# Kernel tuning notes

Measured on AMD Instinct MI355X. Metric: run time of the kernel, lower is better.

The kernel has to match this reference:

```python
import jax, jax.numpy as jnp
import numpy as np

jax.config.update("jax_enable_x64", True)  # module does int64 wraparound hashing

# Derived from BloomFilter(num_items=10_000_000, false_positive_rate=0.01):
#   pre-round num_bits = ceil(1e7 * ln(100) / ln(2)^2) ~= 95,850,584
#   num_hashes = ceil(pre_round_bits / 1e7 * ln(2)) = 7
#   num_bits rounded up to power of two -> 2**27
NUM_BITS = 2 ** 27
BIT_MASK = NUM_BITS - 1
NUM_HASHES = 7
PRIME = 2654435761


def _hash(values):
    """(N,) int64 -> (N, k) bit positions. Matches torch: (v*PRIME + seed) & bit_mask
    (note Python precedence: & binds looser than +). int64 overflow wraps identically."""
    seeds = jnp.arange(NUM_HASHES, dtype=jnp.int64)
    return (values[:, None] * PRIME + seeds[None, :]) & BIT_MASK


def setup_inputs() -> dict:
    key = jax.random.key(0)
    k1, k2 = jax.random.split(key)
    add_values = jax.random.randint(k1, (4_000_000,), 0, 2**31 - 1, dtype=jnp.int64)
    query_values = jax.random.randint(k2, (8_000_000,), 0, 2**31 - 1, dtype=jnp.int64)
    return {"add_values": add_values, "query_values": query_values}


def reference(add_values, query_values):
    # Bit array of NUM_BITS bools. Semantically identical to the packed int64
    # bitset: word w, offset b in torch <-> flat index (w << 6) | b here, and a
    # bitwise-OR of single-bit masks is exactly an idempotent set-True scatter.
    bits = jnp.zeros((NUM_BITS,), dtype=bool)

    # add(): scatter-set all k hash positions of every inserted value
    add_pos = _hash(add_values)  # (M, k)
    bits = bits.at[add_pos.reshape(-1)].set(True)

    # contains(): gather k bits per query and AND-reduce
    q_pos = _hash(query_values)  # (N, k)
    return jnp.all(bits[q_pos], axis=1)  # (N,) bool
```

## Files before the change

### kernel.cpp

```cpp
#include <hip/hip_runtime.h>
#include <stdint.h>


#define NUM_BITS_LOG2 27
#define NUM_BITS (1u << NUM_BITS_LOG2)
#define BIT_MASK (NUM_BITS - 1u)
#define NUM_WORDS (NUM_BITS >> 6)
#define WORD_MASK (NUM_WORDS - 1u)
#define PRIME 2654435761u
#define H_WORDS (NUM_WORDS >> 2)

#define NBUCKETS 512
#define BKT_SHIFT (NUM_BITS_LOG2 - 9)
#define REGION_WORDS (1u << (BKT_SHIFT - 6))
#define H_WORDS_PER_REGION (REGION_WORDS / 4)
#define CAP 8688u
#define CHUNK 8192u

typedef int vint4 __attribute__((ext_vector_type(4)));
typedef unsigned long long vull2 __attribute__((ext_vector_type(2)));

#define WS_H_ONLY 20971520ull
#define WS_FULL   38766592ull

__global__ __launch_bounds__(512) void init_gcnt_kernel(uint32_t* __restrict__ gcnt) {
    gcnt[threadIdx.x] = 0u;
}

__global__ __launch_bounds__(512) void scatter_kernel(
    const int* __restrict__ vals, int n,
    uint32_t* __restrict__ lists, uint32_t* __restrict__ gcnt)
{
    __shared__ uint32_t hist[NBUCKETS];
    __shared__ uint32_t cur[NBUCKETS];
    __shared__ uint32_t gdelta[NBUCKETS];
    __shared__ uint32_t wsum[8];
    __shared__ uint32_t wexc[8];
    __shared__ uint32_t total_s;
    __shared__ uint32_t sortbuf[CHUNK];
    const uint32_t tid = threadIdx.x;
    const uint32_t lane = tid & 63u;
    const uint32_t wv = tid >> 6;
    const uint32_t un = (uint32_t)n;
    const uint32_t nchunks = (un + CHUNK - 1u) / CHUNK;

    for (uint32_t c = blockIdx.x; c < nchunks; c += gridDim.x) {
        const uint32_t base = c * CHUNK;
        const bool full = (base + CHUNK <= un);

        hist[tid] = 0u;
        __syncthreads();

        vint4 vv[4];
        if (full) {
            const vint4* src = (const vint4*)(vals + base);
            #pragma unroll
            for (int k = 0; k < 4; ++k) vv[k] = src[(uint32_t)k * 512u + tid];
            #pragma unroll
            for (int k = 0; k < 4; ++k) {
                #pragma unroll
                for (int j = 0; j < 4; ++j) {
                    uint32_t p = ((uint32_t)vv[k][j] * PRIME) & BIT_MASK;
                    uint32_t b1 = p >> BKT_SHIFT;
                    atomicAdd(&hist[b1], 1u);
                    uint32_t b2 = ((p + 6u) & BIT_MASK) >> BKT_SHIFT;
                    if (b2 != b1) {
                        uint32_t s2 = atomicAdd(&gcnt[b2], 1u);
                        if (s2 < CAP) lists[b2 * CAP + s2] = p;
                    }
                }
            }
        } else {
            #pragma unroll
            for (int k = 0; k < 16; ++k) {
                uint32_t idx = base + (uint32_t)k * 512u + tid;
                if (idx < un) {
                    uint32_t p = ((uint32_t)vals[idx] * PRIME) & BIT_MASK;
                    uint32_t b1 = p >> BKT_SHIFT;
                    atomicAdd(&hist[b1], 1u);
                    uint32_t b2 = ((p + 6u) & BIT_MASK) >> BKT_SHIFT;
                    if (b2 != b1) {
                        uint32_t s2 = atomicAdd(&gcnt[b2], 1u);
                        if (s2 < CAP) lists[b2 * CAP + s2] = p;
                    }
                }
            }
        }
        __syncthreads();

        const uint32_t c0 = hist[tid];
        uint32_t x = c0;
        #pragma unroll
        for (uint32_t d = 1; d < 64; d <<= 1) {
            uint32_t y = __shfl_up(x, d, 64);
            if (lane >= d) x += y;
        }
        if (lane == 63u) wsum[wv] = x;
        __syncthreads();
        if (wv == 0) {
            uint32_t t8 = (lane < 8u) ? wsum[lane] : 0u;
            #pragma unroll
            for (uint32_t d = 1; d < 8; d <<= 1) {
                uint32_t y = __shfl_up(t8, d, 64);
                if (lane >= d) t8 += y;
            }
            if (lane < 8u) wexc[lane] = t8 - wsum[lane];
        }
        __syncthreads();
        const uint32_t inc = x + wexc[wv];
        const uint32_t lb = inc - c0;
        if (tid == NBUCKETS - 1) total_s = inc;

        uint32_t go = c0 ? atomicAdd(&gcnt[tid], c0) : 0u;
        cur[tid] = lb;
        gdelta[tid] = tid * CAP + go - lb;
        __syncthreads();

        if (full) {
            #pragma unroll
            for (int k = 0; k < 4; ++k) {
                #pragma unroll
                for (int j = 0; j < 4; ++j) {
                    uint32_t p = ((uint32_t)vv[k][j] * PRIME) & BIT_MASK;
                    uint32_t b1 = p >> BKT_SHIFT;
                    uint32_t s = atomicAdd(&cur[b1], 1u);
                    sortbuf[s] = p;
                }
            }
        } else {
            #pragma unroll
            for (int k = 0; k < 16; ++k) {
                uint32_t idx = base + (uint32_t)k * 512u + tid;
                if (idx < un) {
                    uint32_t p = ((uint32_t)vals[idx] * PRIME) & BIT_MASK;
                    uint32_t b1 = p >> BKT_SHIFT;
                    uint32_t s = atomicAdd(&cur[b1], 1u);
                    sortbuf[s] = p;
                }
            }
        }
        __syncthreads();

        const uint32_t total = total_s;
        for (uint32_t i = tid; i < total; i += 512u) {
            uint32_t p = sortbuf[i];
            uint32_t b = p >> BKT_SHIFT;
            uint32_t dst = gdelta[b] + i;
            if (dst - b * CAP < CAP) lists[dst] = p;
        }
        __syncthreads();
    }
}

__device__ __forceinline__ void set_window(unsigned long long* bm, uint32_t p, uint32_t b) {
    int d = (int)((p - (b << BKT_SHIFT)) & BIT_MASK);
    if (d >= (1 << 26)) d -= (1 << 27);
    if (d < -6 || d >= (1 << BKT_SHIFT)) return;
    if (d < 0) {
        atomicOr(&bm[0], 0x7Full >> (uint32_t)(-d));
    } else {
        uint32_t w = (uint32_t)d >> 6, s = (uint32_t)d & 63u;
        atomicOr(&bm[w], 0x7Full << s);
        if (s > 57u) atomicOr(&bm[w + 1], 0x7Full >> (64u - s));
    }
}

__device__ __forceinline__ unsigned long long nib16(unsigned long long a) {
    unsigned long long t = a & (a >> 1);
    unsigned long long u = t & (t >> 2);
    u &= 0x1111111111111111ull;
    u |= u >> 3;  u &= 0x0303030303030303ull;
    u |= u >> 6;  u &= 0x000F000F000F000Full;
    u |= u >> 12; u &= 0x000000FF000000FFull;
    u |= u >> 24; return u & 0xFFFFull;
}

__global__ __launch_bounds__(512) void build_bitmap_kernel(
    const uint32_t* __restrict__ lists, const uint32_t* __restrict__ gcnt,
    unsigned long long* __restrict__ bits, unsigned long long* __restrict__ H)
{
    __shared__ unsigned long long bm[REGION_WORDS + 1];
    const uint32_t b = blockIdx.x, tid = threadIdx.x;
    for (uint32_t i = tid; i < REGION_WORDS + 1; i += 512) bm[i] = 0ull;
    __syncthreads();

    const uint32_t m = min(gcnt[b], CAP);
    const uint32_t base = b * CAP;
    for (uint32_t i = tid; i < m; i += 512) set_window(bm, lists[base + i], b);
    __syncthreads();

    const uint32_t out_base = b * REGION_WORDS;
    for (uint32_t i = tid; i < REGION_WORDS / 2; i += 512) {
        vull2 w; w[0] = bm[i * 2]; w[1] = bm[i * 2 + 1];
        *((vull2*)(bits + out_base) + i) = w;
    }
    const uint32_t h_base = b * H_WORDS_PER_REGION;
    for (uint32_t i = tid; i < H_WORDS_PER_REGION; i += 512) {
        unsigned long long hw = nib16(bm[i * 4])
                              | (nib16(bm[i * 4 + 1]) << 16)
                              | (nib16(bm[i * 4 + 2]) << 32)
                              | (nib16(bm[i * 4 + 3]) << 48);
        H[h_base + i] = hw;
    }
}

__device__ __forceinline__ int query_one_branchy(uint32_t v,
                                                 const unsigned long long* __restrict__ bits) {
    uint32_t p = (v * PRIME) & BIT_MASK;
    uint32_t w = p >> 6, s = p & 63u;
    unsigned long long lo = bits[w];
    unsigned long long win;
    if (s <= 57u) win = lo >> s;
    else win = (lo >> s) | (bits[(w + 1u) & WORD_MASK] << (64u - s));
    return ((win & 0x7Full) == 0x7Full) ? 1 : 0;
}

__global__ __launch_bounds__(256, 4) void query_kernelH(
    const int* __restrict__ vals, int n,
    const unsigned long long* __restrict__ bits,
    const uint32_t* __restrict__ H32, int* __restrict__ out)
{
    int t = blockIdx.x * 256 + threadIdx.x;
    int base = t * 16;
    if (base + 15 < n) {
        vint4 v[4];
        #pragma unroll
        for (int k = 0; k < 4; ++k)
            v[k] = __builtin_nontemporal_load((const vint4*)(vals + base) + k);
        uint32_t p[16];
        #pragma unroll
        for (int k = 0; k < 4; ++k)
            #pragma unroll
            for (int j = 0; j < 4; ++j)
                p[k * 4 + j] = ((uint32_t)v[k][j] * PRIME) & BIT_MASK;
        uint32_t pb = 0u;
        #pragma unroll
        for (int j = 0; j < 16; ++j) {
            uint32_t m = ((p[j] + 3u) & BIT_MASK) >> 2;
            pb |= ((H32[m >> 5] >> (m & 31u)) & 1u) << j;
        }
        unsigned long long lo[16], hi[16];
        #pragma unroll
        for (int j = 0; j < 16; ++j) {
            lo[j] = 0ull; hi[j] = 0ull;
            if ((pb >> j) & 1u) lo[j] = bits[p[j] >> 6];
        }
        #pragma unroll
        for (int j = 0; j < 16; ++j) {
            if (((pb >> j) & 1u) && (p[j] & 63u) > 57u)
                hi[j] = bits[((p[j] >> 6) + 1u) & WORD_MASK];
        }
        #pragma unroll
        for (int k = 0; k < 4; ++k) {
            vint4 r;
            #pragma unroll
            for (int j = 0; j < 4; ++j) {
                uint32_t s = p[k * 4 + j] & 63u;
                unsigned long long win = (lo[k * 4 + j] >> s)
                                       | ((hi[k * 4 + j] << 1) << (63u - s));
                r[j] = ((win & 0x7Full) == 0x7Full) ? 1 : 0;
            }
            __builtin_nontemporal_store(r, (vint4*)(out + base) + k);
        }
    } else {
        for (int j = base; j < n; ++j)
            out[j] = query_one_branchy((uint32_t)vals[j], bits);
    }
}

__global__ __launch_bounds__(256) void zero_bits_kernel(vull2* __restrict__ bits, int n2) {
    int i = blockIdx.x * 256 + threadIdx.x;
    if (i < n2) { vull2 z = {0ull, 0ull}; __builtin_nontemporal_store(z, &bits[i]); }
}

__device__ __forceinline__ void insert_one_atomic(uint32_t v,
                                                  unsigned long long* __restrict__ bits) {
    uint32_t p = (v * PRIME) & BIT_MASK;
    uint32_t w = p >> 6, s = p & 63u;
    atomicOr(bits + w, 0x7Full << s);
    if (s > 57u) atomicOr(bits + ((w + 1u) & WORD_MASK), 0x7Full >> (64u - s));
}

__global__ __launch_bounds__(256) void insert_atomic_kernel(const int* __restrict__ vals, int n,
                                                            unsigned long long* __restrict__ bits) {
    int t = blockIdx.x * 256 + threadIdx.x;
    int base = t * 4;
    if (base + 3 < n) {
        vint4 v = __builtin_nontemporal_load((const vint4*)vals + t);
        insert_one_atomic((uint32_t)v.x, bits);
        insert_one_atomic((uint32_t)v.y, bits);
        insert_one_atomic((uint32_t)v.z, bits);
        insert_one_atomic((uint32_t)v.w, bits);
    } else {
        for (int j = base; j < n; ++j) insert_one_atomic((uint32_t)vals[j], bits);
    }
}

__global__ __launch_bounds__(256) void build_h_kernel(
    const unsigned long long* __restrict__ bits, unsigned long long* __restrict__ H)
{
    uint32_t i = blockIdx.x * 256 + threadIdx.x;
    const vull2* b2 = (const vull2*)bits + (size_t)i * 2;
    vull2 a = b2[0];
    vull2 b = b2[1];
    unsigned long long hw = nib16(a[0])
                          | (nib16(a[1]) << 16)
                          | (nib16(b[0]) << 32)
                          | (nib16(b[1]) << 48);
    H[i] = hw;
}

__global__ __launch_bounds__(256) void query_kernel8(
    const int* __restrict__ vals, int n,
    const unsigned long long* __restrict__ bits, int* __restrict__ out)
{
    int t = blockIdx.x * 256 + threadIdx.x;
    int base = t * 8;
    if (base + 7 < n) {
        vint4 v0 = __builtin_nontemporal_load((const vint4*)(vals + base));
        vint4 v1 = __builtin_nontemporal_load((const vint4*)(vals + base + 4));
        vint4 r0, r1;
        #pragma unroll
        for (int j = 0; j < 8; ++j) {
            uint32_t v = (uint32_t)(j < 4 ? v0[j] : v1[j - 4]);
            int r = query_one_branchy(v, bits);
            if (j < 4) r0[j] = r; else r1[j - 4] = r;
        }
        __builtin_nontemporal_store(r0, (vint4*)(out + base));
        __builtin_nontemporal_store(r1, (vint4*)(out + base + 4));
    } else {
        for (int j = base; j < n; ++j)
            out[j] = query_one_branchy((uint32_t)vals[j], bits);
    }
}

extern "C" void kernel_launch(void* const* d_in, const int* in_sizes, int n_in,
                              void* d_out, int out_size, void* d_ws, size_t ws_size,
                              hipStream_t stream) {
    const int* add_values   = (const int*)d_in[0];
    const int* query_values = (const int*)d_in[1];
    const int n_add   = in_sizes[0];
    const int n_query = in_sizes[1];
    int* out = (int*)d_out;

    uint8_t* ws = (uint8_t*)d_ws;
    unsigned long long* bits = (unsigned long long*)ws;
    unsigned long long* H    = (unsigned long long*)(ws + 16777216);
    uint32_t* lists = (uint32_t*)(ws + 20971520);
    uint32_t* gcnt  = (uint32_t*)(ws + 38764544);

    if (ws_size >= WS_FULL) {
        const uint32_t nchunks = ((uint32_t)n_add + CHUNK - 1u) / CHUNK;
        init_gcnt_kernel<<<1, 512, 0, stream>>>(gcnt);
        scatter_kernel<<<nchunks, 512, 0, stream>>>(add_values, n_add, lists, gcnt);
        build_bitmap_kernel<<<NBUCKETS, 512, 0, stream>>>(lists, gcnt, bits, H);
        const int threads16 = (n_query + 15) / 16;
        query_kernelH<<<(threads16 + 255) / 256, 256, 0, stream>>>(
            query_values, n_query, bits, (const uint32_t*)H, out);
    } else if (ws_size >= WS_H_ONLY) {
        const int n2 = NUM_WORDS / 2;
        zero_bits_kernel<<<(n2 + 255) / 256, 256, 0, stream>>>((vull2*)bits, n2);
        const int threads4 = (n_add + 3) / 4;
        insert_atomic_kernel<<<(threads4 + 255) / 256, 256, 0, stream>>>(
            add_values, n_add, bits);
        build_h_kernel<<<H_WORDS / 256, 256, 0, stream>>>(bits, H);
        const int threads16 = (n_query + 15) / 16;
        query_kernelH<<<(threads16 + 255) / 256, 256, 0, stream>>>(
            query_values, n_query, bits, (const uint32_t*)H, out);
    } else {
        const int n2 = NUM_WORDS / 2;
        zero_bits_kernel<<<(n2 + 255) / 256, 256, 0, stream>>>((vull2*)bits, n2);
        const int threads4 = (n_add + 3) / 4;
        insert_atomic_kernel<<<(threads4 + 255) / 256, 256, 0, stream>>>(
            add_values, n_add, bits);
        const int threads8 = (n_query + 7) / 8;
        query_kernel8<<<(threads8 + 255) / 256, 256, 0, stream>>>(
            query_values, n_query, bits, out);
    }
}
```

Measured before the change: 196.4 us.

## Split bitmap build into half-regions, shrink scatter chunks, batch query loads

The bitmap build now runs two blocks per bucket, each covering half of the region. This halves the shared-memory bitmap per block and doubles the block count, so more blocks can be resident at once. The cost is that each list is read twice and filtered by sub-range. The scatter chunk size is halved to 4096, which doubles the number of chunk blocks and their global counter atomics. The query kernel issues its gathers in two groups of 8 instead of 16, lowering register pressure at the cost of less memory-level parallelism per thread.

```diff
diff --git a/kernel.cpp b/kernel.cpp
--- a/kernel.cpp
+++ b/kernel.cpp
@@ -14,8 +14,11 @@
 #define BKT_SHIFT (NUM_BITS_LOG2 - 9)
 #define REGION_WORDS (1u << (BKT_SHIFT - 6))
 #define H_WORDS_PER_REGION (REGION_WORDS / 4)
+#define SUB_SHIFT (BKT_SHIFT - 1)
+#define SUB_WORDS (1u << (SUB_SHIFT - 6))
+#define SUB_H (SUB_WORDS / 4)
 #define CAP 8688u
-#define CHUNK 8192u
+#define CHUNK 4096u
 
 typedef int vint4 __attribute__((ext_vector_type(4)));
 typedef unsigned long long vull2 __attribute__((ext_vector_type(2)));
@@ -51,13 +54,13 @@
         hist[tid] = 0u;
         __syncthreads();
 
-        vint4 vv[4];
+        vint4 vv[2];
         if (full) {
             const vint4* src = (const vint4*)(vals + base);
             #pragma unroll
-            for (int k = 0; k < 4; ++k) vv[k] = src[(uint32_t)k * 512u + tid];
-            #pragma unroll
-            for (int k = 0; k < 4; ++k) {
+            for (int k = 0; k < 2; ++k) vv[k] = src[(uint32_t)k * 512u + tid];
+            #pragma unroll
+            for (int k = 0; k < 2; ++k) {
                 #pragma unroll
                 for (int j = 0; j < 4; ++j) {
                     uint32_t p = ((uint32_t)vv[k][j] * PRIME) & BIT_MASK;
@@ -72,7 +75,7 @@
             }
         } else {
             #pragma unroll
-            for (int k = 0; k < 16; ++k) {
+            for (int k = 0; k < 8; ++k) {
                 uint32_t idx = base + (uint32_t)k * 512u + tid;
                 if (idx < un) {
                     uint32_t p = ((uint32_t)vals[idx] * PRIME) & BIT_MASK;
@@ -118,7 +121,7 @@
 
         if (full) {
             #pragma unroll
-            for (int k = 0; k < 4; ++k) {
+            for (int k = 0; k < 2; ++k) {
                 #pragma unroll
                 for (int j = 0; j < 4; ++j) {
                     uint32_t p = ((uint32_t)vv[k][j] * PRIME) & BIT_MASK;
@@ -129,7 +132,7 @@
             }
         } else {
             #pragma unroll
-            for (int k = 0; k < 16; ++k) {
+            for (int k = 0; k < 8; ++k) {
                 uint32_t idx = base + (uint32_t)k * 512u + tid;
                 if (idx < un) {
                     uint32_t p = ((uint32_t)vals[idx] * PRIME) & BIT_MASK;
@@ -152,10 +155,11 @@
     }
 }
 
-__device__ __forceinline__ void set_window(unsigned long long* bm, uint32_t p, uint32_t b) {
-    int d = (int)((p - (b << BKT_SHIFT)) & BIT_MASK);
+__device__ __forceinline__ void set_window_sub(unsigned long long* bm, uint32_t p,
+                                               uint32_t sub_base) {
+    int d = (int)((p - sub_base) & BIT_MASK);
     if (d >= (1 << 26)) d -= (1 << 27);
-    if (d < -6 || d >= (1 << BKT_SHIFT)) return;
+    if (d < -6 || d >= (1 << SUB_SHIFT)) return;
     if (d < 0) {
         atomicOr(&bm[0], 0x7Full >> (uint32_t)(-d));
     } else {
@@ -179,23 +183,26 @@
     const uint32_t* __restrict__ lists, const uint32_t* __restrict__ gcnt,
     unsigned long long* __restrict__ bits, unsigned long long* __restrict__ H)
 {
-    __shared__ unsigned long long bm[REGION_WORDS + 1];
-    const uint32_t b = blockIdx.x, tid = threadIdx.x;
-    for (uint32_t i = tid; i < REGION_WORDS + 1; i += 512) bm[i] = 0ull;
+    __shared__ unsigned long long bm[SUB_WORDS + 1];
+    const uint32_t b = blockIdx.x >> 1;
+    const uint32_t half = blockIdx.x & 1u;
+    const uint32_t tid = threadIdx.x;
+    const uint32_t sub_base = (b << BKT_SHIFT) + (half << SUB_SHIFT);
+    for (uint32_t i = tid; i < SUB_WORDS + 1; i += 512) bm[i] = 0ull;
     __syncthreads();
 
     const uint32_t m = min(gcnt[b], CAP);
     const uint32_t base = b * CAP;
-    for (uint32_t i = tid; i < m; i += 512) set_window(bm, lists[base + i], b);
+    for (uint32_t i = tid; i < m; i += 512) set_window_sub(bm, lists[base + i], sub_base);
     __syncthreads();
 
-    const uint32_t out_base = b * REGION_WORDS;
-    for (uint32_t i = tid; i < REGION_WORDS / 2; i += 512) {
+    const uint32_t out_base = b * REGION_WORDS + half * SUB_WORDS;
+    for (uint32_t i = tid; i < SUB_WORDS / 2; i += 512) {
         vull2 w; w[0] = bm[i * 2]; w[1] = bm[i * 2 + 1];
         *((vull2*)(bits + out_base) + i) = w;
     }
-    const uint32_t h_base = b * H_WORDS_PER_REGION;
-    for (uint32_t i = tid; i < H_WORDS_PER_REGION; i += 512) {
+    const uint32_t h_base = b * H_WORDS_PER_REGION + half * SUB_H;
+    for (uint32_t i = tid; i < SUB_H; i += 512) {
         unsigned long long hw = nib16(bm[i * 4])
                               | (nib16(bm[i * 4 + 1]) << 16)
                               | (nib16(bm[i * 4 + 2]) << 32)
@@ -239,28 +246,34 @@
             uint32_t m = ((p[j] + 3u) & BIT_MASK) >> 2;
             pb |= ((H32[m >> 5] >> (m & 31u)) & 1u) << j;
         }
-        unsigned long long lo[16], hi[16];
-        #pragma unroll
-        for (int j = 0; j < 16; ++j) {
-            lo[j] = 0ull; hi[j] = 0ull;
-            if ((pb >> j) & 1u) lo[j] = bits[p[j] >> 6];
-        }
-        #pragma unroll
-        for (int j = 0; j < 16; ++j) {
-            if (((pb >> j) & 1u) && (p[j] & 63u) > 57u)
-                hi[j] = bits[((p[j] >> 6) + 1u) & WORD_MASK];
-        }
-        #pragma unroll
-        for (int k = 0; k < 4; ++k) {
-            vint4 r;
-            #pragma unroll
-            for (int j = 0; j < 4; ++j) {
-                uint32_t s = p[k * 4 + j] & 63u;
-                unsigned long long win = (lo[k * 4 + j] >> s)
-                                       | ((hi[k * 4 + j] << 1) << (63u - s));
-                r[j] = ((win & 0x7Full) == 0x7Full) ? 1 : 0;
-            }
-            __builtin_nontemporal_store(r, (vint4*)(out + base) + k);
+        #pragma unroll
+        for (int h = 0; h < 2; ++h) {
+            unsigned long long lo[8], hi[8];
+            #pragma unroll
+            for (int j = 0; j < 8; ++j) {
+                const int idx = h * 8 + j;
+                lo[j] = 0ull; hi[j] = 0ull;
+                if ((pb >> idx) & 1u) lo[j] = bits[p[idx] >> 6];
+            }
+            #pragma unroll
+            for (int j = 0; j < 8; ++j) {
+                const int idx = h * 8 + j;
+                if (((pb >> idx) & 1u) && (p[idx] & 63u) > 57u)
+                    hi[j] = bits[((p[idx] >> 6) + 1u) & WORD_MASK];
+            }
+            #pragma unroll
+            for (int k = 0; k < 2; ++k) {
+                vint4 r;
+                #pragma unroll
+                for (int j = 0; j < 4; ++j) {
+                    const int idx = h * 8 + k * 4 + j;
+                    uint32_t s = p[idx] & 63u;
+                    unsigned long long win = (lo[k * 4 + j] >> s)
+                                           | ((hi[k * 4 + j] << 1) << (63u - s));
+                    r[j] = ((win & 0x7Full) == 0x7Full) ? 1 : 0;
+                }
+                __builtin_nontemporal_store(r, (vint4*)(out + base) + h * 2 + k);
+            }
         }
     } else {
         for (int j = base; j < n; ++j)
@@ -353,7 +366,7 @@
         const uint32_t nchunks = ((uint32_t)n_add + CHUNK - 1u) / CHUNK;
         init_gcnt_kernel<<<1, 512, 0, stream>>>(gcnt);
         scatter_kernel<<<nchunks, 512, 0, stream>>>(add_values, n_add, lists, gcnt);
-        build_bitmap_kernel<<<NBUCKETS, 512, 0, stream>>>(lists, gcnt, bits, H);
+        build_bitmap_kernel<<<NBUCKETS * 2, 512, 0, stream>>>(lists, gcnt, bits, H);
         const int threads16 = (n_query + 15) / 16;
         query_kernelH<<<(threads16 + 255) / 256, 256, 0, stream>>>(
             query_values, n_query, bits, (const uint32_t*)H, out);
```

Result: slower. 201.0 us (+2.3%).

## Replace 4-bit summary filter with 2-bit-granularity H2 prefilter built in separate kernel

Applied to the files above, without the earlier changes.

Replaces the coarse summary bitmap H (one bit per aligned 4-bit group of ones) with an 8 MB H2 bitmap holding one bit per pair of adjacent set bits. Each query checks three consecutive H2 bits before touching the full bitmap. H2 is built by a separate kernel and overlaid on the lists workspace region, freeing workspace. The query kernel drops from 16 to 8 items per thread and removes the occupancy hint. The finer prefilter should reject more queries early, at the cost of a larger summary that fits less well in cache, plus an extra kernel launch and another full pass over the bitmap.

```diff
diff --git a/kernel.cpp b/kernel.cpp
--- a/kernel.cpp
+++ b/kernel.cpp
@@ -8,20 +8,21 @@
 #define NUM_WORDS (NUM_BITS >> 6)
 #define WORD_MASK (NUM_WORDS - 1u)
 #define PRIME 2654435761u
-#define H_WORDS (NUM_WORDS >> 2)
+
+#define H2_WORDS (1u << 20)
+#define H2_WMASK (H2_WORDS - 1u)
 
 #define NBUCKETS 512
 #define BKT_SHIFT (NUM_BITS_LOG2 - 9)
 #define REGION_WORDS (1u << (BKT_SHIFT - 6))
-#define H_WORDS_PER_REGION (REGION_WORDS / 4)
 #define CAP 8688u
 #define CHUNK 8192u
 
 typedef int vint4 __attribute__((ext_vector_type(4)));
 typedef unsigned long long vull2 __attribute__((ext_vector_type(2)));
 
-#define WS_H_ONLY 20971520ull
-#define WS_FULL   38766592ull
+#define WS_H2_ONLY 25165824ull
+#define WS_FULL    34572288ull
 
 __global__ __launch_bounds__(512) void init_gcnt_kernel(uint32_t* __restrict__ gcnt) {
     gcnt[threadIdx.x] = 0u;
@@ -165,19 +166,9 @@
     }
 }
 
-__device__ __forceinline__ unsigned long long nib16(unsigned long long a) {
-    unsigned long long t = a & (a >> 1);
-    unsigned long long u = t & (t >> 2);
-    u &= 0x1111111111111111ull;
-    u |= u >> 3;  u &= 0x0303030303030303ull;
-    u |= u >> 6;  u &= 0x000F000F000F000Full;
-    u |= u >> 12; u &= 0x000000FF000000FFull;
-    u |= u >> 24; return u & 0xFFFFull;
-}
-
 __global__ __launch_bounds__(512) void build_bitmap_kernel(
     const uint32_t* __restrict__ lists, const uint32_t* __restrict__ gcnt,
-    unsigned long long* __restrict__ bits, unsigned long long* __restrict__ H)
+    unsigned long long* __restrict__ bits)
 {
     __shared__ unsigned long long bm[REGION_WORDS + 1];
     const uint32_t b = blockIdx.x, tid = threadIdx.x;
@@ -194,14 +185,25 @@
         vull2 w; w[0] = bm[i * 2]; w[1] = bm[i * 2 + 1];
         *((vull2*)(bits + out_base) + i) = w;
     }
-    const uint32_t h_base = b * H_WORDS_PER_REGION;
-    for (uint32_t i = tid; i < H_WORDS_PER_REGION; i += 512) {
-        unsigned long long hw = nib16(bm[i * 4])
-                              | (nib16(bm[i * 4 + 1]) << 16)
-                              | (nib16(bm[i * 4 + 2]) << 32)
-                              | (nib16(bm[i * 4 + 3]) << 48);
-        H[h_base + i] = hw;
-    }
+}
+
+__device__ __forceinline__ unsigned long long compact32(unsigned long long a) {
+    unsigned long long t = a & (a >> 1);
+    unsigned long long x = t & 0x5555555555555555ull;
+    x = (x | (x >> 1))  & 0x3333333333333333ull;
+    x = (x | (x >> 2))  & 0x0F0F0F0F0F0F0F0Full;
+    x = (x | (x >> 4))  & 0x00FF00FF00FF00FFull;
+    x = (x | (x >> 8))  & 0x0000FFFF0000FFFFull;
+    x = (x | (x >> 16)) & 0x00000000FFFFFFFFull;
+    return x;
+}
+
+__global__ __launch_bounds__(256) void build_h2_kernel(
+    const unsigned long long* __restrict__ bits, unsigned long long* __restrict__ H2)
+{
+    uint32_t i = blockIdx.x * 256 + threadIdx.x;
+    vull2 a = *((const vull2*)bits + i);
+    H2[i] = compact32(a[0]) | (compact32(a[1]) << 32);
 }
 
 __device__ __forceinline__ int query_one_branchy(uint32_t v,
@@ -215,53 +217,59 @@
     return ((win & 0x7Full) == 0x7Full) ? 1 : 0;
 }
 
-__global__ __launch_bounds__(256, 4) void query_kernelH(
+__global__ __launch_bounds__(256) void query_kernelH2(
     const int* __restrict__ vals, int n,
     const unsigned long long* __restrict__ bits,
-    const uint32_t* __restrict__ H32, int* __restrict__ out)
+    const unsigned long long* __restrict__ H2, int* __restrict__ out)
 {
     int t = blockIdx.x * 256 + threadIdx.x;
-    int base = t * 16;
-    if (base + 15 < n) {
-        vint4 v[4];
-        #pragma unroll
-        for (int k = 0; k < 4; ++k)
-            v[k] = __builtin_nontemporal_load((const vint4*)(vals + base) + k);
-        uint32_t p[16];
-        #pragma unroll
-        for (int k = 0; k < 4; ++k)
-            #pragma unroll
-            for (int j = 0; j < 4; ++j)
-                p[k * 4 + j] = ((uint32_t)v[k][j] * PRIME) & BIT_MASK;
-        uint32_t pb = 0u;
-        #pragma unroll
-        for (int j = 0; j < 16; ++j) {
-            uint32_t m = ((p[j] + 3u) & BIT_MASK) >> 2;
-            pb |= ((H32[m >> 5] >> (m & 31u)) & 1u) << j;
-        }
-        unsigned long long lo[16], hi[16];
-        #pragma unroll
-        for (int j = 0; j < 16; ++j) {
+    int base = t * 8;
+    if (base + 7 < n) {
+        vint4 v0 = __builtin_nontemporal_load((const vint4*)(vals + base));
+        vint4 v1 = __builtin_nontemporal_load((const vint4*)(vals + base + 4));
+        uint32_t p[8], q0[8], sh[8];
+        #pragma unroll
+        for (int j = 0; j < 4; ++j) {
+            p[j]     = ((uint32_t)v0[j] * PRIME) & BIT_MASK;
+            p[j + 4] = ((uint32_t)v1[j] * PRIME) & BIT_MASK;
+        }
+        unsigned long long hh[8];
+        #pragma unroll
+        for (int j = 0; j < 8; ++j) {
+            q0[j] = ((p[j] + 1u) & BIT_MASK) >> 1;
+            sh[j] = q0[j] & 63u;
+            hh[j] = H2[q0[j] >> 6];
+        }
+        uint32_t pass[8];
+        #pragma unroll
+        for (int j = 0; j < 8; ++j) {
+            uint32_t trip = (uint32_t)(hh[j] >> sh[j]);
+            if (sh[j] > 61u)
+                trip |= (uint32_t)(H2[((q0[j] >> 6) + 1u) & H2_WMASK] << (64u - sh[j]));
+            pass[j] = ((trip & 7u) == 7u);
+        }
+        unsigned long long lo[8], hi[8];
+        uint32_t w[8], s[8];
+        #pragma unroll
+        for (int j = 0; j < 8; ++j) {
+            w[j] = p[j] >> 6; s[j] = p[j] & 63u;
             lo[j] = 0ull; hi[j] = 0ull;
-            if ((pb >> j) & 1u) lo[j] = bits[p[j] >> 6];
-        }
-        #pragma unroll
-        for (int j = 0; j < 16; ++j) {
-            if (((pb >> j) & 1u) && (p[j] & 63u) > 57u)
-                hi[j] = bits[((p[j] >> 6) + 1u) & WORD_MASK];
-        }
-        #pragma unroll
-        for (int k = 0; k < 4; ++k) {
-            vint4 r;
-            #pragma unroll
-            for (int j = 0; j < 4; ++j) {
-                uint32_t s = p[k * 4 + j] & 63u;
-                unsigned long long win = (lo[k * 4 + j] >> s)
-                                       | ((hi[k * 4 + j] << 1) << (63u - s));
-                r[j] = ((win & 0x7Full) == 0x7Full) ? 1 : 0;
-            }
-            __builtin_nontemporal_store(r, (vint4*)(out + base) + k);
-        }
+            if (pass[j]) lo[j] = bits[w[j]];
+        }
+        #pragma unroll
+        for (int j = 0; j < 8; ++j) {
+            if (pass[j] && s[j] > 57u)
+                hi[j] = bits[(w[j] + 1u) & WORD_MASK];
+        }
+        vint4 r0, r1;
+        #pragma unroll
+        for (int j = 0; j < 8; ++j) {
+            unsigned long long win = (lo[j] >> s[j]) | ((hi[j] << 1) << (63u - s[j]));
+            int r = ((win & 0x7Full) == 0x7Full) ? 1 : 0;
+            if (j < 4) r0[j] = r; else r1[j - 4] = r;
+        }
+        __builtin_nontemporal_store(r0, (vint4*)(out + base));
+        __builtin_nontemporal_store(r1, (vint4*)(out + base + 4));
     } else {
         for (int j = base; j < n; ++j)
             out[j] = query_one_branchy((uint32_t)vals[j], bits);
@@ -296,20 +304,6 @@
     }
 }
 
-__global__ __launch_bounds__(256) void build_h_kernel(
-    const unsigned long long* __restrict__ bits, unsigned long long* __restrict__ H)
-{
-    uint32_t i = blockIdx.x * 256 + threadIdx.x;
-    const vull2* b2 = (const vull2*)bits + (size_t)i * 2;
-    vull2 a = b2[0];
-    vull2 b = b2[1];
-    unsigned long long hw = nib16(a[0])
-                          | (nib16(a[1]) << 16)
-                          | (nib16(b[0]) << 32)
-                          | (nib16(b[1]) << 48);
-    H[i] = hw;
-}
-
 __global__ __launch_bounds__(256) void query_kernel8(
     const int* __restrict__ vals, int n,
     const unsigned long long* __restrict__ bits, int* __restrict__ out)
@@ -345,35 +339,35 @@
 
     uint8_t* ws = (uint8_t*)d_ws;
     unsigned long long* bits = (unsigned long long*)ws;
-    unsigned long long* H    = (unsigned long long*)(ws + 16777216);
-    uint32_t* lists = (uint32_t*)(ws + 20971520);
-    uint32_t* gcnt  = (uint32_t*)(ws + 38764544);
+    uint32_t* lists = (uint32_t*)(ws + 16777216);
+    uint32_t* gcnt  = (uint32_t*)(ws + 34570240);
+    unsigned long long* H2 = (unsigned long long*)(ws + 16777216);
+
+    const int threads8 = (n_query + 7) / 8;
 
     if (ws_size >= WS_FULL) {
         const uint32_t nchunks = ((uint32_t)n_add + CHUNK - 1u) / CHUNK;
         init_gcnt_kernel<<<1, 512, 0, stream>>>(gcnt);
         scatter_kernel<<<nchunks, 512, 0, stream>>>(add_values, n_add, lists, gcnt);
-        build_bitmap_kernel<<<NBUCKETS, 512, 0, stream>>>(lists, gcnt, bits, H);
-        const int threads16 = (n_query + 15) / 16;
-        query_kernelH<<<(threads16 + 255) / 256, 256, 0, stream>>>(
-            query_values, n_query, bits, (const uint32_t*)H, out);
-    } else if (ws_size >= WS_H_ONLY) {
+        build_bitmap_kernel<<<NBUCKETS, 512, 0, stream>>>(lists, gcnt, bits);
+        build_h2_kernel<<<H2_WORDS / 256, 256, 0, stream>>>(bits, H2);
+        query_kernelH2<<<(threads8 + 255) / 256, 256, 0, stream>>>(
+            query_values, n_query, bits, H2, out);
+    } else if (ws_size >= WS_H2_ONLY) {
         const int n2 = NUM_WORDS / 2;
         zero_bits_kernel<<<(n2 + 255) / 256, 256, 0, stream>>>((vull2*)bits, n2);
         const int threads4 = (n_add + 3) / 4;
         insert_atomic_kernel<<<(threads4 + 255) / 256, 256, 0, stream>>>(
             add_values, n_add, bits);
-        build_h_kernel<<<H_WORDS / 256, 256, 0, stream>>>(bits, H);
-        const int threads16 = (n_query + 15) / 16;
-        query_kernelH<<<(threads16 + 255) / 256, 256, 0, stream>>>(
-            query_values, n_query, bits, (const uint32_t*)H, out);
+        build_h2_kernel<<<H2_WORDS / 256, 256, 0, stream>>>(bits, H2);
+        query_kernelH2<<<(threads8 + 255) / 256, 256, 0, stream>>>(
+            query_values, n_query, bits, H2, out);
     } else {
         const int n2 = NUM_WORDS / 2;
         zero_bits_kernel<<<(n2 + 255) / 256, 256, 0, stream>>>((vull2*)bits, n2);
         const int threads4 = (n_add + 3) / 4;
         insert_atomic_kernel<<<(threads4 + 255) / 256, 256, 0, stream>>>(
             add_values, n_add, bits);
-        const int threads8 = (n_query + 7) / 8;
         query_kernel8<<<(threads8 + 255) / 256, 256, 0, stream>>>(
             query_values, n_query, bits, out);
     }
```

After: 214.6 us. 9.3% more time.
